# Kernel optimization log

Hardware: AMD Instinct MI355X
Metric: run time of the kernel (lower is better)

Reference implementation:

```python
import jax, jax.numpy as jnp
import numpy as np

KS, STRIDE, DIL = 5, 1, 1
PAD = (KS + (KS - 1) * (DIL - 1) - 1) // 2
EPS = 1e-5


def _unfold_t(x):
    # x: (N, C, T, V) -> (N, C, T_out, KS, V), zero-padded temporal windows
    N, C, T, V = x.shape
    xp = jnp.pad(x, ((0, 0), (0, 0), (PAD, PAD), (0, 0)))
    t_out = (T + 2 * PAD - DIL * (KS - 1) - 1) // STRIDE + 1
    idx = jnp.arange(t_out)[:, None] * STRIDE + jnp.arange(KS)[None, :] * DIL  # (T_out, KS)
    return xp[:, :, idx, :]


def _bn2d(x, g, b):
    # training-mode BatchNorm2d: biased batch stats over (N, T, V)
    mu = jnp.mean(x, axis=(0, 2, 3), keepdims=True)
    var = jnp.var(x, axis=(0, 2, 3), keepdims=True)
    xn = (x - mu) * jax.lax.rsqrt(var + EPS)
    return xn * g[None, :, None, None] + b[None, :, None, None]


def setup_inputs() -> dict:
    key = jax.random.key(0)
    ks = jax.random.split(key, 8)
    N, C, T, V = 64, 64, 128, 25
    R, O = 8, 128
    s = 0.05
    return {
        "x": jax.random.normal(ks[0], (N, C, T, V), jnp.float32),
        "Wv": jax.random.normal(ks[1], (R, C), jnp.float32) * s,
        "bv": jax.random.normal(ks[2], (R,), jnp.float32) * s,
        "Ww": jax.random.normal(ks[3], (KS * KS, KS), jnp.float32) * s,
        "bw": jax.random.normal(ks[4], (KS * KS,), jnp.float32) * s,
        "g_bn": jnp.ones((R,), jnp.float32),
        "b_bn": jnp.zeros((R,), jnp.float32),
        "Wr": jax.random.normal(ks[5], (R, C), jnp.float32) * s,
        "br": jax.random.normal(ks[6], (R,), jnp.float32) * s,
        "g_r": jnp.ones((R,), jnp.float32),
        "b_r": jnp.zeros((R,), jnp.float32),
        "Wo": jax.random.normal(ks[7], (O, R), jnp.float32) * s,
        "bo": jnp.zeros((O,), jnp.float32),
        "g_o": jnp.ones((O,), jnp.float32),
        "b_o": jnp.zeros((O,), jnp.float32),
    }


def reference(x, Wv, bv, Ww, bw, g_bn, b_bn, Wr, br, g_r, b_r, Wo, bo, g_o, b_o):
    N, C, T, V = x.shape
    # convV (1x1) then unfold both x and v
    v0 = jnp.einsum('rc,nctv->nrtv', Wv, x) + bv[None, :, None, None]
    xu = _unfold_t(x)      # (N, C, T, W, V)
    vu = _unfold_t(v0)     # (N, R, T, W, V)
    # mean over channels, move window dim to channel position for convW
    m = jnp.mean(xu, axis=1).transpose(0, 2, 1, 3)  # (N, W, T, V)
    w = jnp.einsum('ow,nwtv->notv', Ww, m) + bw[None, :, None, None]
    weights = jnp.tanh(w.reshape(N, KS, KS, T, V))  # (N, W, W, T, V)
    att = jnp.einsum('nwutv,nctuv->nctv', weights, vu)  # (N, R, T, V)
    # residual 1x1 conv + BN (in_channels != out_channels -> conv path)
    res = _bn2d(jnp.einsum('rc,nctv->nrtv', Wr, x) + br[None, :, None, None], g_r, b_r)
    h = _bn2d(att, g_bn, b_bn) + res
    h = jnp.where(h >= 0, h, 0.1 * h)  # LeakyReLU(0.1)
    out = _bn2d(jnp.einsum('or,nrtv->notv', Wo, h) + bo[None, :, None, None], g_o, b_o)
    return out
```

## Files before the change

### kernel.cpp

```cpp
#include <hip/hip_runtime.h>
#include <math.h>

#define TV 3200
#define NTV 204800
#define NB 800
constexpr float EPSF = 1e-5f;

template<int NS>
__device__ inline void write_partials(float (&vals)[NS], float* __restrict__ out, float* lds){
  int lane = threadIdx.x & 63;
  int wid  = threadIdx.x >> 6;
  #pragma unroll
  for (int s = 0; s < NS; ++s){
    float v = vals[s];
    #pragma unroll
    for (int o = 32; o > 0; o >>= 1) v += __shfl_down(v, o);
    if (lane == 0) lds[s*4 + wid] = v;
  }
  __syncthreads();
  if ((int)threadIdx.x < NS){
    float v = lds[threadIdx.x*4+0] + lds[threadIdx.x*4+1]
            + lds[threadIdx.x*4+2] + lds[threadIdx.x*4+3];
    out[threadIdx.x*NB + blockIdx.x] = v;
  }
}

__global__ __launch_bounds__(256) void k_proj(const float* __restrict__ x,
    const float* __restrict__ Wv, const float* __restrict__ bv,
    const float* __restrict__ Wr, const float* __restrict__ br,
    float* __restrict__ v0, float* __restrict__ r0, float* __restrict__ s,
    float* __restrict__ pr){
  __shared__ float sWv[512], sWr[512], lds[16*4];
  int tid = threadIdx.x;
  for (int i = tid; i < 512; i += 256){ sWv[i] = Wv[i]; sWr[i] = Wr[i]; }
  __syncthreads();
  int p = blockIdx.x*256 + tid;
  int n = p / TV, tv = p - n*TV;
  const float* xp = x + (size_t)n*64*TV + tv;
  float av[8] = {0,0,0,0,0,0,0,0};
  float ar[8] = {0,0,0,0,0,0,0,0};
  float ssum = 0.f;
  for (int c = 0; c < 64; ++c){
    float xv = xp[(size_t)c*TV];
    ssum += xv;
    #pragma unroll
    for (int r = 0; r < 8; ++r){
      av[r] = fmaf(sWv[r*64+c], xv, av[r]);
      ar[r] = fmaf(sWr[r*64+c], xv, ar[r]);
    }
  }
  s[p] = ssum * 0.015625f;
  float* v0p = v0 + (size_t)n*8*TV + tv;
  float* r0p = r0 + (size_t)n*8*TV + tv;
  float vals[16];
  #pragma unroll
  for (int r = 0; r < 8; ++r){
    v0p[(size_t)r*TV] = av[r] + bv[r];
    float rr = ar[r] + br[r];
    r0p[(size_t)r*TV] = rr;
    vals[r] = rr; vals[8+r] = rr*rr;
  }
  write_partials<16>(vals, pr, lds);
}

__global__ __launch_bounds__(256) void k_w2(const float* __restrict__ s,
    const float* __restrict__ Ww, const float* __restrict__ bw,
    float* __restrict__ W2){
  __shared__ float sWw[125], sbw[25];
  int tid = threadIdx.x;
  if (tid < 125) sWw[tid] = Ww[tid];
  if (tid < 25)  sbw[tid] = bw[tid];
  __syncthreads();
  int p = blockIdx.x*256 + tid;
  int n = p / TV, tv = p - n*TV;
  int t = tv / 25, v = tv - t*25;
  float m[5];
  #pragma unroll
  for (int k = 0; k < 5; ++k){
    int tt = t + k - 2;
    m[k] = (tt >= 0 && tt < 128) ? s[n*TV + tt*25 + v] : 0.f;
  }
  float w2[5] = {0,0,0,0,0};
  #pragma unroll
  for (int w = 0; w < 5; ++w){
    #pragma unroll
    for (int u = 0; u < 5; ++u){
      int o = w*5 + u;
      float wo = sbw[o];
      #pragma unroll
      for (int k = 0; k < 5; ++k) wo = fmaf(sWw[o*5+k], m[k], wo);
      w2[u] += tanhf(wo);
    }
  }
  float* W2p = W2 + (size_t)n*5*TV + tv;
  #pragma unroll
  for (int u = 0; u < 5; ++u) W2p[(size_t)u*TV] = w2[u];
}

__global__ __launch_bounds__(256) void k_att(const float* __restrict__ W2,
    const float* __restrict__ v0, float* __restrict__ att, float* __restrict__ patt){
  __shared__ float lds[16*4];
  int tid = threadIdx.x;
  int p = blockIdx.x*256 + tid;
  int n = p / TV, tv = p - n*TV;
  int t = tv / 25, v = tv - t*25;
  float a[8] = {0,0,0,0,0,0,0,0};
  const float* W2p = W2 + (size_t)n*5*TV + tv;
  const float* v0n = v0 + (size_t)n*8*TV;
  #pragma unroll
  for (int u = 0; u < 5; ++u){
    int tt = t + u - 2;
    if (tt >= 0 && tt < 128){
      float wu = W2p[(size_t)u*TV];
      const float* vp = v0n + tt*25 + v;
      #pragma unroll
      for (int r = 0; r < 8; ++r) a[r] = fmaf(wu, vp[(size_t)r*TV], a[r]);
    }
  }
  float* ap = att + (size_t)n*8*TV + tv;
  float vals[16];
  #pragma unroll
  for (int r = 0; r < 8; ++r){
    ap[(size_t)r*TV] = a[r];
    vals[r] = a[r]; vals[8+r] = a[r]*a[r];
  }
  write_partials<16>(vals, patt, lds);
}

__global__ __launch_bounds__(256) void k_bncoef(const float* __restrict__ pr,
    const float* __restrict__ patt,
    const float* __restrict__ g_bn, const float* __restrict__ b_bn,
    const float* __restrict__ g_r, const float* __restrict__ b_r,
    float* __restrict__ coef){
  __shared__ float lds[8];
  int b = blockIdx.x;
  bool isatt = (b >= 8);
  int r = isatt ? b - 8 : b;
  const float* ps = (isatt ? patt : pr) + r*NB;
  const float* pq = (isatt ? patt : pr) + (8+r)*NB;
  float s1 = 0.f, s2 = 0.f;
  for (int i = threadIdx.x; i < NB; i += 256){ s1 += ps[i]; s2 += pq[i]; }
  int lane = threadIdx.x & 63, wid = threadIdx.x >> 6;
  #pragma unroll
  for (int o = 32; o > 0; o >>= 1){ s1 += __shfl_down(s1, o); s2 += __shfl_down(s2, o); }
  if (lane == 0){ lds[wid] = s1; lds[4+wid] = s2; }
  __syncthreads();
  if (threadIdx.x == 0){
    float sum = lds[0]+lds[1]+lds[2]+lds[3];
    float sq  = lds[4]+lds[5]+lds[6]+lds[7];
    float mu  = sum / (float)NTV;
    float var = sq / (float)NTV - mu*mu;
    float g  = isatt ? g_bn[r] : g_r[r];
    float bb = isatt ? b_bn[r] : b_r[r];
    float a = g * rsqrtf(var + EPSF);
    float c = bb - a*mu;
    int base = isatt ? 0 : 16;
    coef[base + r] = a;
    coef[base + 8 + r] = c;
  }
}

__global__ __launch_bounds__(256) void k_h(const float* __restrict__ att,
    const float* __restrict__ r0, const float* __restrict__ coef,
    float* __restrict__ h, float* __restrict__ ph){
  __shared__ float lds[44*4];
  __shared__ float sc[32];
  int tid = threadIdx.x;
  if (tid < 32) sc[tid] = coef[tid];
  __syncthreads();
  int p = blockIdx.x*256 + tid;
  int n = p / TV, tv = p - n*TV;
  const float* ap = att + (size_t)n*8*TV + tv;
  const float* rp = r0  + (size_t)n*8*TV + tv;
  float* hp = h + (size_t)n*8*TV + tv;
  float hv[8];
  #pragma unroll
  for (int r = 0; r < 8; ++r){
    float z = sc[r]*ap[(size_t)r*TV] + sc[8+r] + sc[16+r]*rp[(size_t)r*TV] + sc[24+r];
    hv[r] = (z >= 0.f) ? z : 0.1f*z;
    hp[(size_t)r*TV] = hv[r];
  }
  float vals[44];
  #pragma unroll
  for (int r = 0; r < 8; ++r) vals[r] = hv[r];
  int cnt = 8;
  #pragma unroll
  for (int r = 0; r < 8; ++r){
    #pragma unroll
    for (int r2 = r; r2 < 8; ++r2) vals[cnt++] = hv[r]*hv[r2];
  }
  write_partials<44>(vals, ph, lds);
}

__global__ __launch_bounds__(256) void k_hred(const float* __restrict__ ph,
    float* __restrict__ hstat){
  __shared__ float lds[4];
  int j = blockIdx.x;
  float s1 = 0.f;
  for (int i = threadIdx.x; i < NB; i += 256) s1 += ph[j*NB + i];
  int lane = threadIdx.x & 63, wid = threadIdx.x >> 6;
  #pragma unroll
  for (int o = 32; o > 0; o >>= 1) s1 += __shfl_down(s1, o);
  if (lane == 0) lds[wid] = s1;
  __syncthreads();
  if (threadIdx.x == 0) hstat[j] = lds[0]+lds[1]+lds[2]+lds[3];
}

__global__ __launch_bounds__(128) void k_fold(const float* __restrict__ hstat,
    const float* __restrict__ Wo, const float* __restrict__ bo,
    const float* __restrict__ g_o, const float* __restrict__ b_o,
    float* __restrict__ fold, float* __restrict__ bfold){
  __shared__ double muh[8];
  __shared__ double exx[8][8];
  int o = threadIdx.x;
  if (o < 8) muh[o] = (double)hstat[o] / (double)NTV;
  if (o == 0){
    int cnt = 8;
    for (int r = 0; r < 8; ++r)
      for (int r2 = r; r2 < 8; ++r2){
        double e = (double)hstat[cnt++] / (double)NTV;
        exx[r][r2] = e; exx[r2][r] = e;
      }
  }
  __syncthreads();
  double w[8];
  for (int r = 0; r < 8; ++r) w[r] = (double)Wo[o*8+r];
  double bob = (double)bo[o];
  double mu = bob;
  for (int r = 0; r < 8; ++r) mu += w[r]*muh[r];
  double t = 0.0;
  for (int r = 0; r < 8; ++r)
    for (int r2 = 0; r2 < 8; ++r2) t += w[r]*w[r2]*exx[r][r2];
  double ey2 = t + 2.0*bob*(mu - bob) + bob*bob;
  double var = ey2 - mu*mu;
  double a = (double)g_o[o] / sqrt(var + (double)EPSF);
  for (int r = 0; r < 8; ++r) fold[o*8+r] = (float)(a * w[r]);
  bfold[o] = (float)(a * (bob - mu) + (double)b_o[o]);
}

__global__ __launch_bounds__(256) void k_out(const float* __restrict__ h,
    const float* __restrict__ fold, const float* __restrict__ bfold,
    float* __restrict__ out){
  __shared__ float sW[1024], sB[128];
  int tid = threadIdx.x;
  for (int i = tid; i < 1024; i += 256) sW[i] = fold[i];
  if (tid < 128) sB[tid] = bfold[tid];
  __syncthreads();
  int p = blockIdx.x*256 + tid;
  int n = p / TV, tv = p - n*TV;
  const float* hp = h + (size_t)n*8*TV + tv;
  float hv[8];
  #pragma unroll
  for (int r = 0; r < 8; ++r) hv[r] = hp[(size_t)r*TV];
  float* op = out + (size_t)n*128*TV + tv;
  #pragma unroll 4
  for (int o = 0; o < 128; ++o){
    float y = sB[o];
    #pragma unroll
    for (int r = 0; r < 8; ++r) y = fmaf(sW[o*8+r], hv[r], y);
    op[(size_t)o*TV] = y;
  }
}

extern "C" void kernel_launch(void* const* d_in, const int* in_sizes, int n_in,
                              void* d_out, int out_size, void* d_ws, size_t ws_size,
                              hipStream_t stream){
  const float* x    = (const float*)d_in[0];
  const float* Wv   = (const float*)d_in[1];
  const float* bv   = (const float*)d_in[2];
  const float* Ww   = (const float*)d_in[3];
  const float* bw   = (const float*)d_in[4];
  const float* g_bn = (const float*)d_in[5];
  const float* b_bn = (const float*)d_in[6];
  const float* Wr   = (const float*)d_in[7];
  const float* br   = (const float*)d_in[8];
  const float* g_r  = (const float*)d_in[9];
  const float* b_r  = (const float*)d_in[10];
  const float* Wo   = (const float*)d_in[11];
  const float* bo   = (const float*)d_in[12];
  const float* g_o  = (const float*)d_in[13];
  const float* b_o  = (const float*)d_in[14];

  float* ws = (float*)d_ws;
  size_t off = 0;
  float* v0   = ws + off; off += 1638400;
  float* r0   = ws + off; off += 1638400;
  float* s    = ws + off; off += 204800;
  float* W2   = ws + off; off += 1024000;
  float* att  = ws + off; off += 1638400;
  float* hbuf = ws + off; off += 1638400;
  float* pr   = ws + off; off += 16*NB;
  float* patt = ws + off; off += 16*NB;
  float* ph   = ws + off; off += 44*NB;
  float* coef = ws + off; off += 32;
  float* hstat= ws + off; off += 44;
  float* fold = ws + off; off += 1024;
  float* bfold= ws + off; off += 128;

  k_proj  <<<NB, 256, 0, stream>>>(x, Wv, bv, Wr, br, v0, r0, s, pr);
  k_w2    <<<NB, 256, 0, stream>>>(s, Ww, bw, W2);
  k_att   <<<NB, 256, 0, stream>>>(W2, v0, att, patt);
  k_bncoef<<<16, 256, 0, stream>>>(pr, patt, g_bn, b_bn, g_r, b_r, coef);
  k_h     <<<NB, 256, 0, stream>>>(att, r0, coef, hbuf, ph);
  k_hred  <<<44, 256, 0, stream>>>(ph, hstat);
  k_fold  <<<1, 128, 0, stream>>>(hstat, Wo, bo, g_o, b_o, fold, bfold);
  k_out   <<<NB, 256, 0, stream>>>(hbuf, fold, bfold, (float*)d_out);
}
```

Before: 240.7 us.

## Fuse all stages into one cooperative persistent kernel with grid syncs

Replaces the chain of eight kernel launches with a single cooperative kernel of 400 blocks, each thread handling two positions. Grid-wide barriers separate the stats phases, and the r0, att and h intermediates stay in registers instead of round-tripping through global memory. The W2 computation is also fused into the attention step, which removes the W2 buffer. The cost is three grid.syncs and a serial BN-coefficient recompute in every block; if the cooperative launch fails, the code falls back to the multi-kernel path, with k_w2 now merged into k_att.

```diff
diff --git a/kernel.cpp b/kernel.cpp
--- a/kernel.cpp
+++ b/kernel.cpp
@@ -1,27 +1,247 @@
 #include <hip/hip_runtime.h>
+#include <hip/hip_cooperative_groups.h>
 #include <math.h>
+
+namespace cg = cooperative_groups;
 
 #define TV 3200
 #define NTV 204800
-#define NB 800
+#define NBC 400
+#define NBF 800
 constexpr float EPSF = 1e-5f;
 
+struct Params {
+  const float *x, *Wv, *bv, *Ww, *bw, *g_bn, *b_bn, *Wr, *br, *g_r, *b_r, *Wo, *bo, *g_o, *b_o;
+  float *v0, *s, *pr, *patt, *ph, *out;
+};
+
 template<int NS>
-__device__ inline void write_partials(float (&vals)[NS], float* __restrict__ out, float* lds){
+__device__ inline void partials(const float (&vals)[NS], float* lds, float* out, int ncols){
   int lane = threadIdx.x & 63;
   int wid  = threadIdx.x >> 6;
   #pragma unroll
-  for (int s = 0; s < NS; ++s){
-    float v = vals[s];
+  for (int j = 0; j < NS; ++j){
+    float v = vals[j];
     #pragma unroll
     for (int o = 32; o > 0; o >>= 1) v += __shfl_down(v, o);
-    if (lane == 0) lds[s*4 + wid] = v;
+    if (lane == 0) lds[j*4 + wid] = v;
   }
   __syncthreads();
   if ((int)threadIdx.x < NS){
-    float v = lds[threadIdx.x*4+0] + lds[threadIdx.x*4+1]
-            + lds[threadIdx.x*4+2] + lds[threadIdx.x*4+3];
-    out[threadIdx.x*NB + blockIdx.x] = v;
+    out[threadIdx.x*ncols + blockIdx.x] =
+      lds[threadIdx.x*4+0] + lds[threadIdx.x*4+1] + lds[threadIdx.x*4+2] + lds[threadIdx.x*4+3];
+  }
+  __syncthreads();
+}
+
+__global__ __launch_bounds__(256, 2) void mega(Params P){
+  cg::grid_group grid = cg::this_grid();
+  __shared__ __align__(16) float smem[1536];
+  const int tid = threadIdx.x;
+  int p[2], nn[2], tv[2], tt_[2], vv[2];
+  p[0] = blockIdx.x*512 + tid;
+  p[1] = p[0] + 256;
+  #pragma unroll
+  for (int q = 0; q < 2; ++q){
+    nn[q] = p[q] / TV; tv[q] = p[q] - nn[q]*TV;
+    tt_[q] = tv[q] / 25; vv[q] = tv[q] - tt_[q]*25;
+  }
+
+  for (int i = tid; i < 512; i += 256){ smem[i] = P.Wv[i]; smem[512+i] = P.Wr[i]; }
+  __syncthreads();
+  float av[2][8] = {}, ar[2][8] = {}, ss[2] = {0.f, 0.f};
+  const float* xp[2];
+  #pragma unroll
+  for (int q = 0; q < 2; ++q) xp[q] = P.x + (size_t)nn[q]*64*TV + tv[q];
+  for (int c = 0; c < 64; ++c){
+    #pragma unroll
+    for (int q = 0; q < 2; ++q){
+      float xv = xp[q][(size_t)c*TV];
+      ss[q] += xv;
+      #pragma unroll
+      for (int r = 0; r < 8; ++r){
+        av[q][r] = fmaf(smem[r*64+c], xv, av[q][r]);
+        ar[q][r] = fmaf(smem[512+r*64+c], xv, ar[q][r]);
+      }
+    }
+  }
+  float r0r[2][8];
+  {
+    float vals[16];
+    #pragma unroll
+    for (int q = 0; q < 2; ++q){
+      P.s[p[q]] = ss[q] * 0.015625f;
+      float* v0p = P.v0 + (size_t)nn[q]*8*TV + tv[q];
+      #pragma unroll
+      for (int r = 0; r < 8; ++r){
+        v0p[(size_t)r*TV] = av[q][r] + P.bv[r];
+        r0r[q][r] = ar[q][r] + P.br[r];
+      }
+    }
+    #pragma unroll
+    for (int r = 0; r < 8; ++r){
+      vals[r]   = r0r[0][r] + r0r[1][r];
+      vals[8+r] = r0r[0][r]*r0r[0][r] + r0r[1][r]*r0r[1][r];
+    }
+    __syncthreads();
+    partials<16>(vals, smem, P.pr, NBC);
+  }
+  __threadfence();
+  grid.sync();
+  __threadfence();
+
+  if (tid < 125) smem[1280+tid] = P.Ww[tid];
+  if (tid < 25)  smem[1408+tid] = P.bw[tid];
+  __syncthreads();
+  float attr[2][8] = {};
+  #pragma unroll
+  for (int q = 0; q < 2; ++q){
+    float m[5];
+    #pragma unroll
+    for (int k = 0; k < 5; ++k){
+      int tt = tt_[q] + k - 2;
+      m[k] = (tt >= 0 && tt < 128) ? P.s[nn[q]*TV + tt*25 + vv[q]] : 0.f;
+    }
+    const float* v0n = P.v0 + (size_t)nn[q]*8*TV;
+    #pragma unroll
+    for (int u = 0; u < 5; ++u){
+      float w2u = 0.f;
+      #pragma unroll
+      for (int w = 0; w < 5; ++w){
+        int o = w*5 + u;
+        float acc = smem[1408+o];
+        #pragma unroll
+        for (int k = 0; k < 5; ++k) acc = fmaf(smem[1280+o*5+k], m[k], acc);
+        w2u += tanhf(acc);
+      }
+      int tt = tt_[q] + u - 2;
+      if (tt >= 0 && tt < 128){
+        const float* vp = v0n + tt*25 + vv[q];
+        #pragma unroll
+        for (int r = 0; r < 8; ++r) attr[q][r] = fmaf(w2u, vp[(size_t)r*TV], attr[q][r]);
+      }
+    }
+  }
+  {
+    float vals[16];
+    #pragma unroll
+    for (int r = 0; r < 8; ++r){
+      vals[r]   = attr[0][r] + attr[1][r];
+      vals[8+r] = attr[0][r]*attr[0][r] + attr[1][r]*attr[1][r];
+    }
+    __syncthreads();
+    partials<16>(vals, smem, P.patt, NBC);
+  }
+  __threadfence();
+  grid.sync();
+  __threadfence();
+
+  {
+    int ch = tid >> 4, chunk = tid & 15;
+    const float* base = (ch >= 8) ? P.patt : P.pr;
+    int r = ch & 7;
+    const float* ps = base + r*NBC + chunk*25;
+    const float* pq = base + (8+r)*NBC + chunk*25;
+    float s1 = 0.f, s2 = 0.f;
+    for (int i = 0; i < 25; ++i){ s1 += ps[i]; s2 += pq[i]; }
+    smem[tid] = s1; smem[256+tid] = s2;
+    __syncthreads();
+    if (tid < 16){
+      float sum = 0.f, sq = 0.f;
+      #pragma unroll
+      for (int i = 0; i < 16; ++i){ sum += smem[tid*16+i]; sq += smem[256+tid*16+i]; }
+      float mu  = sum / (float)NTV;
+      float var = sq / (float)NTV - mu*mu;
+      bool isatt = (tid >= 8); int rr = tid & 7;
+      float g  = isatt ? P.g_bn[rr] : P.g_r[rr];
+      float bb = isatt ? P.b_bn[rr] : P.b_r[rr];
+      float a  = g * rsqrtf(var + EPSF);
+      int b0 = isatt ? 512 : 528;
+      smem[b0+rr] = a; smem[b0+8+rr] = bb - a*mu;
+    }
+    __syncthreads();
+  }
+
+  float hv[2][8];
+  #pragma unroll
+  for (int q = 0; q < 2; ++q)
+    #pragma unroll
+    for (int r = 0; r < 8; ++r){
+      float z = smem[512+r]*attr[q][r] + smem[520+r] + smem[528+r]*r0r[q][r] + smem[536+r];
+      hv[q][r] = (z >= 0.f) ? z : 0.1f*z;
+    }
+  {
+    float vals[44];
+    #pragma unroll
+    for (int r = 0; r < 8; ++r) vals[r] = hv[0][r] + hv[1][r];
+    int cnt = 8;
+    #pragma unroll
+    for (int r = 0; r < 8; ++r)
+      #pragma unroll
+      for (int r2 = r; r2 < 8; ++r2){
+        vals[cnt++] = hv[0][r]*hv[0][r2] + hv[1][r]*hv[1][r2];
+      }
+    __syncthreads();
+    partials<44>(vals, smem, P.ph, NBC);
+  }
+  __threadfence();
+  grid.sync();
+  __threadfence();
+
+  {
+    if (tid < 176){
+      int j = tid >> 2, qk = tid & 3;
+      const float* row = P.ph + j*NBC + qk*100;
+      float acc = 0.f;
+      for (int i = 0; i < 100; ++i) acc += row[i];
+      smem[tid] = acc;
+    }
+    __syncthreads();
+    if (tid < 44)
+      smem[1200+tid] = smem[4*tid]+smem[4*tid+1]+smem[4*tid+2]+smem[4*tid+3];
+    __syncthreads();
+    double* muh = (double*)(smem + 1248);
+    double* exx = (double*)(smem + 1264);
+    if (tid < 8) muh[tid] = (double)smem[1200+tid] / (double)NTV;
+    if (tid == 0){
+      int cnt = 8;
+      for (int r = 0; r < 8; ++r)
+        for (int r2 = r; r2 < 8; ++r2){
+          double e = (double)smem[1200+cnt] / (double)NTV; cnt++;
+          exx[r*8+r2] = e; exx[r2*8+r] = e;
+        }
+    }
+    __syncthreads();
+    if (tid < 128){
+      double w[8];
+      #pragma unroll
+      for (int r = 0; r < 8; ++r) w[r] = (double)P.Wo[tid*8+r];
+      double bob = (double)P.bo[tid];
+      double mu = bob;
+      for (int r = 0; r < 8; ++r) mu += w[r]*muh[r];
+      double t2 = 0.0;
+      for (int r = 0; r < 8; ++r)
+        for (int r2 = 0; r2 < 8; ++r2) t2 += w[r]*w[r2]*exx[r*8+r2];
+      double ey2 = t2 + 2.0*bob*(mu - bob) + bob*bob;
+      double var = ey2 - mu*mu;
+      double a = (double)P.g_o[tid] / sqrt(var + (double)EPSF);
+      #pragma unroll
+      for (int r = 0; r < 8; ++r) smem[tid*8+r] = (float)(a * w[r]);
+      smem[1024+tid] = (float)(a * (bob - mu) + (double)P.b_o[tid]);
+    }
+    __syncthreads();
+  }
+
+  #pragma unroll
+  for (int q = 0; q < 2; ++q){
+    float* op = P.out + (size_t)nn[q]*128*TV + tv[q];
+    #pragma unroll 4
+    for (int o = 0; o < 128; ++o){
+      float y = smem[1024+o];
+      #pragma unroll
+      for (int r = 0; r < 8; ++r) y = fmaf(smem[o*8+r], hv[q][r], y);
+      op[(size_t)o*TV] = y;
+    }
   }
 }
 
@@ -37,8 +257,7 @@
   int p = blockIdx.x*256 + tid;
   int n = p / TV, tv = p - n*TV;
   const float* xp = x + (size_t)n*64*TV + tv;
-  float av[8] = {0,0,0,0,0,0,0,0};
-  float ar[8] = {0,0,0,0,0,0,0,0};
+  float av[8] = {}, ar[8] = {};
   float ssum = 0.f;
   for (int c = 0; c < 64; ++c){
     float xv = xp[(size_t)c*TV];
@@ -60,13 +279,13 @@
     r0p[(size_t)r*TV] = rr;
     vals[r] = rr; vals[8+r] = rr*rr;
   }
-  write_partials<16>(vals, pr, lds);
-}
-
-__global__ __launch_bounds__(256) void k_w2(const float* __restrict__ s,
+  partials<16>(vals, lds, pr, NBF);
+}
+
+__global__ __launch_bounds__(256) void k_att(const float* __restrict__ s,
     const float* __restrict__ Ww, const float* __restrict__ bw,
-    float* __restrict__ W2){
-  __shared__ float sWw[125], sbw[25];
+    const float* __restrict__ v0, float* __restrict__ att, float* __restrict__ patt){
+  __shared__ float sWw[125], sbw[25], lds[16*4];
   int tid = threadIdx.x;
   if (tid < 125) sWw[tid] = Ww[tid];
   if (tid < 25)  sbw[tid] = bw[tid];
@@ -80,41 +299,24 @@
     int tt = t + k - 2;
     m[k] = (tt >= 0 && tt < 128) ? s[n*TV + tt*25 + v] : 0.f;
   }
-  float w2[5] = {0,0,0,0,0};
-  #pragma unroll
-  for (int w = 0; w < 5; ++w){
-    #pragma unroll
-    for (int u = 0; u < 5; ++u){
+  float a[8] = {};
+  const float* v0n = v0 + (size_t)n*8*TV;
+  #pragma unroll
+  for (int u = 0; u < 5; ++u){
+    float w2u = 0.f;
+    #pragma unroll
+    for (int w = 0; w < 5; ++w){
       int o = w*5 + u;
-      float wo = sbw[o];
-      #pragma unroll
-      for (int k = 0; k < 5; ++k) wo = fmaf(sWw[o*5+k], m[k], wo);
-      w2[u] += tanhf(wo);
-    }
-  }
-  float* W2p = W2 + (size_t)n*5*TV + tv;
-  #pragma unroll
-  for (int u = 0; u < 5; ++u) W2p[(size_t)u*TV] = w2[u];
-}
-
-__global__ __launch_bounds__(256) void k_att(const float* __restrict__ W2,
-    const float* __restrict__ v0, float* __restrict__ att, float* __restrict__ patt){
-  __shared__ float lds[16*4];
-  int tid = threadIdx.x;
-  int p = blockIdx.x*256 + tid;
-  int n = p / TV, tv = p - n*TV;
-  int t = tv / 25, v = tv - t*25;
-  float a[8] = {0,0,0,0,0,0,0,0};
-  const float* W2p = W2 + (size_t)n*5*TV + tv;
-  const float* v0n = v0 + (size_t)n*8*TV;
-  #pragma unroll
-  for (int u = 0; u < 5; ++u){
+      float acc = sbw[o];
+      #pragma unroll
+      for (int k = 0; k < 5; ++k) acc = fmaf(sWw[o*5+k], m[k], acc);
+      w2u += tanhf(acc);
+    }
     int tt = t + u - 2;
     if (tt >= 0 && tt < 128){
-      float wu = W2p[(size_t)u*TV];
       const float* vp = v0n + tt*25 + v;
       #pragma unroll
-      for (int r = 0; r < 8; ++r) a[r] = fmaf(wu, vp[(size_t)r*TV], a[r]);
+      for (int r = 0; r < 8; ++r) a[r] = fmaf(w2u, vp[(size_t)r*TV], a[r]);
     }
   }
   float* ap = att + (size_t)n*8*TV + tv;
@@ -124,7 +326,7 @@
     ap[(size_t)r*TV] = a[r];
     vals[r] = a[r]; vals[8+r] = a[r]*a[r];
   }
-  write_partials<16>(vals, patt, lds);
+  partials<16>(vals, lds, patt, NBF);
 }
 
 __global__ __launch_bounds__(256) void k_bncoef(const float* __restrict__ pr,
@@ -136,10 +338,10 @@
   int b = blockIdx.x;
   bool isatt = (b >= 8);
   int r = isatt ? b - 8 : b;
-  const float* ps = (isatt ? patt : pr) + r*NB;
-  const float* pq = (isatt ? patt : pr) + (8+r)*NB;
+  const float* ps = (isatt ? patt : pr) + r*NBF;
+  const float* pq = (isatt ? patt : pr) + (8+r)*NBF;
   float s1 = 0.f, s2 = 0.f;
-  for (int i = threadIdx.x; i < NB; i += 256){ s1 += ps[i]; s2 += pq[i]; }
+  for (int i = threadIdx.x; i < NBF; i += 256){ s1 += ps[i]; s2 += pq[i]; }
   int lane = threadIdx.x & 63, wid = threadIdx.x >> 6;
   #pragma unroll
   for (int o = 32; o > 0; o >>= 1){ s1 += __shfl_down(s1, o); s2 += __shfl_down(s2, o); }
@@ -153,10 +355,9 @@
     float g  = isatt ? g_bn[r] : g_r[r];
     float bb = isatt ? b_bn[r] : b_r[r];
     float a = g * rsqrtf(var + EPSF);
-    float c = bb - a*mu;
     int base = isatt ? 0 : 16;
     coef[base + r] = a;
-    coef[base + 8 + r] = c;
+    coef[base + 8 + r] = bb - a*mu;
   }
 }
 
@@ -173,23 +374,22 @@
   const float* ap = att + (size_t)n*8*TV + tv;
   const float* rp = r0  + (size_t)n*8*TV + tv;
   float* hp = h + (size_t)n*8*TV + tv;
-  float hv[8];
+  float hvv[8];
   #pragma unroll
   for (int r = 0; r < 8; ++r){
     float z = sc[r]*ap[(size_t)r*TV] + sc[8+r] + sc[16+r]*rp[(size_t)r*TV] + sc[24+r];
-    hv[r] = (z >= 0.f) ? z : 0.1f*z;
-    hp[(size_t)r*TV] = hv[r];
+    hvv[r] = (z >= 0.f) ? z : 0.1f*z;
+    hp[(size_t)r*TV] = hvv[r];
   }
   float vals[44];
   #pragma unroll
-  for (int r = 0; r < 8; ++r) vals[r] = hv[r];
+  for (int r = 0; r < 8; ++r) vals[r] = hvv[r];
   int cnt = 8;
   #pragma unroll
-  for (int r = 0; r < 8; ++r){
-    #pragma unroll
-    for (int r2 = r; r2 < 8; ++r2) vals[cnt++] = hv[r]*hv[r2];
-  }
-  write_partials<44>(vals, ph, lds);
+  for (int r = 0; r < 8; ++r)
+    #pragma unroll
+    for (int r2 = r; r2 < 8; ++r2) vals[cnt++] = hvv[r]*hvv[r2];
+  partials<44>(vals, lds, ph, NBF);
 }
 
 __global__ __launch_bounds__(256) void k_hred(const float* __restrict__ ph,
@@ -197,7 +397,7 @@
   __shared__ float lds[4];
   int j = blockIdx.x;
   float s1 = 0.f;
-  for (int i = threadIdx.x; i < NB; i += 256) s1 += ph[j*NB + i];
+  for (int i = threadIdx.x; i < NBF; i += 256) s1 += ph[j*NBF + i];
   int lane = threadIdx.x & 63, wid = threadIdx.x >> 6;
   #pragma unroll
   for (int o = 32; o > 0; o >>= 1) s1 += __shfl_down(s1, o);
@@ -249,15 +449,15 @@
   int p = blockIdx.x*256 + tid;
   int n = p / TV, tv = p - n*TV;
   const float* hp = h + (size_t)n*8*TV + tv;
-  float hv[8];
-  #pragma unroll
-  for (int r = 0; r < 8; ++r) hv[r] = hp[(size_t)r*TV];
+  float hvv[8];
+  #pragma unroll
+  for (int r = 0; r < 8; ++r) hvv[r] = hp[(size_t)r*TV];
   float* op = out + (size_t)n*128*TV + tv;
   #pragma unroll 4
   for (int o = 0; o < 128; ++o){
     float y = sB[o];
     #pragma unroll
-    for (int r = 0; r < 8; ++r) y = fmaf(sW[o*8+r], hv[r], y);
+    for (int r = 0; r < 8; ++r) y = fmaf(sW[o*8+r], hvv[r], y);
     op[(size_t)o*TV] = y;
   }
 }
@@ -265,44 +465,51 @@
 extern "C" void kernel_launch(void* const* d_in, const int* in_sizes, int n_in,
                               void* d_out, int out_size, void* d_ws, size_t ws_size,
                               hipStream_t stream){
-  const float* x    = (const float*)d_in[0];
-  const float* Wv   = (const float*)d_in[1];
-  const float* bv   = (const float*)d_in[2];
-  const float* Ww   = (const float*)d_in[3];
-  const float* bw   = (const float*)d_in[4];
-  const float* g_bn = (const float*)d_in[5];
-  const float* b_bn = (const float*)d_in[6];
-  const float* Wr   = (const float*)d_in[7];
-  const float* br   = (const float*)d_in[8];
-  const float* g_r  = (const float*)d_in[9];
-  const float* b_r  = (const float*)d_in[10];
-  const float* Wo   = (const float*)d_in[11];
-  const float* bo   = (const float*)d_in[12];
-  const float* g_o  = (const float*)d_in[13];
-  const float* b_o  = (const float*)d_in[14];
-
   float* ws = (float*)d_ws;
   size_t off = 0;
-  float* v0   = ws + off; off += 1638400;
+  Params P;
+  P.x    = (const float*)d_in[0];
+  P.Wv   = (const float*)d_in[1];
+  P.bv   = (const float*)d_in[2];
+  P.Ww   = (const float*)d_in[3];
+  P.bw   = (const float*)d_in[4];
+  P.g_bn = (const float*)d_in[5];
+  P.b_bn = (const float*)d_in[6];
+  P.Wr   = (const float*)d_in[7];
+  P.br   = (const float*)d_in[8];
+  P.g_r  = (const float*)d_in[9];
+  P.b_r  = (const float*)d_in[10];
+  P.Wo   = (const float*)d_in[11];
+  P.bo   = (const float*)d_in[12];
+  P.g_o  = (const float*)d_in[13];
+  P.b_o  = (const float*)d_in[14];
+  P.v0   = ws + off; off += 1638400;
+  P.s    = ws + off; off += 204800;
+  P.pr   = ws + off; off += 16*NBC;
+  P.patt = ws + off; off += 16*NBC;
+  P.ph   = ws + off; off += 44*NBC;
+  P.out  = (float*)d_out;
   float* r0   = ws + off; off += 1638400;
-  float* s    = ws + off; off += 204800;
-  float* W2   = ws + off; off += 1024000;
-  float* att  = ws + off; off += 1638400;
+  float* W2att= ws + off; off += 1638400;
   float* hbuf = ws + off; off += 1638400;
-  float* pr   = ws + off; off += 16*NB;
-  float* patt = ws + off; off += 16*NB;
-  float* ph   = ws + off; off += 44*NB;
+  float* prF  = ws + off; off += 16*NBF;
+  float* pattF= ws + off; off += 16*NBF;
+  float* phF  = ws + off; off += 44*NBF;
   float* coef = ws + off; off += 32;
   float* hstat= ws + off; off += 44;
   float* fold = ws + off; off += 1024;
   float* bfold= ws + off; off += 128;
 
-  k_proj  <<<NB, 256, 0, stream>>>(x, Wv, bv, Wr, br, v0, r0, s, pr);
-  k_w2    <<<NB, 256, 0, stream>>>(s, Ww, bw, W2);
-  k_att   <<<NB, 256, 0, stream>>>(W2, v0, att, patt);
-  k_bncoef<<<16, 256, 0, stream>>>(pr, patt, g_bn, b_bn, g_r, b_r, coef);
-  k_h     <<<NB, 256, 0, stream>>>(att, r0, coef, hbuf, ph);
-  k_hred  <<<44, 256, 0, stream>>>(ph, hstat);
-  k_fold  <<<1, 128, 0, stream>>>(hstat, Wo, bo, g_o, b_o, fold, bfold);
-  k_out   <<<NB, 256, 0, stream>>>(hbuf, fold, bfold, (float*)d_out);
-}
+  void* args[] = { &P };
+  hipError_t err = hipLaunchCooperativeKernel((const void*)mega, dim3(NBC), dim3(256),
+                                              args, 0, stream);
+  if (err != hipSuccess){
+    k_proj  <<<NBF, 256, 0, stream>>>(P.x, P.Wv, P.bv, P.Wr, P.br, P.v0, r0, P.s, prF);
+    k_att   <<<NBF, 256, 0, stream>>>(P.s, P.Ww, P.bw, P.v0, W2att, pattF);
+    k_bncoef<<<16, 256, 0, stream>>>(prF, pattF, P.g_bn, P.b_bn, P.g_r, P.b_r, coef);
+    k_h     <<<NBF, 256, 0, stream>>>(W2att, r0, coef, hbuf, phF);
+    k_hred  <<<44, 256, 0, stream>>>(phF, hstat);
+    k_fold  <<<1, 128, 0, stream>>>(hstat, P.Wo, P.bo, P.g_o, P.b_o, fold, bfold);
+    k_out   <<<NBF, 256, 0, stream>>>(hbuf, fold, bfold, P.out);
+  }
+}
```

After: 571.8 us. +137.5%, slower.
